# Kernel tuning notes

Hardware: AMD Instinct MI355X
Metric: run time of the kernel (lower is better)

## Reference

```python
import jax, jax.numpy as jnp
import numpy as np

EMBED_DIM = 768
NUM_HEADS = 12
HEAD_DIM = EMBED_DIM // NUM_HEADS
KERNEL = 7


def _neighbor_index(size, kernel):
    # NATTEN border-clamped neighborhood: window start = clip(i - k//2, 0, size-k)
    start = np.clip(np.arange(size) - kernel // 2, 0, size - kernel)
    return jnp.asarray(start[:, None] + np.arange(kernel)[None, :])  # [size, kernel]


def setup_inputs() -> dict:
    key = jax.random.key(0)
    k1, k2, k3, k4, k5 = jax.random.split(key, 5)
    B, H, W, C = 8, 64, 64, EMBED_DIM
    x = jax.random.normal(k1, (B, H, W, C), dtype=jnp.float32)
    # torch.nn.Linear layout: weight [out, in]
    w_qkv = jax.random.normal(k2, (3 * C, C), dtype=jnp.float32) * (C ** -0.5)
    b_qkv = jax.random.normal(k3, (3 * C,), dtype=jnp.float32) * 0.02
    w_proj = jax.random.normal(k4, (C, C), dtype=jnp.float32) * (C ** -0.5)
    b_proj = jax.random.normal(k5, (C,), dtype=jnp.float32) * 0.02
    return {"x": x, "w_qkv": w_qkv, "b_qkv": b_qkv, "w_proj": w_proj, "b_proj": b_proj}


def reference(x, w_qkv, b_qkv, w_proj, b_proj):
    B, H, W, C = x.shape
    scale = HEAD_DIM ** -0.5
    qkv = (x @ w_qkv.T + b_qkv).reshape(B, H, W, 3, NUM_HEADS, HEAD_DIM)
    q = qkv[..., 0, :, :] * scale          # [B,H,W,nh,hd]
    k = qkv[..., 1, :, :]
    v = qkv[..., 2, :, :]

    idx_i = _neighbor_index(H, KERNEL)      # [H,K]
    idx_j = _neighbor_index(W, KERNEL)      # [W,K]

    # Logits over the K*K local neighborhood, one shifted gather per offset
    # (avoids materializing [B,H,W,K2,nh,hd]).
    logits = []
    for ki in range(KERNEL):
        k_row = jnp.take(k, idx_i[:, ki], axis=1)          # [B,H,W,nh,hd]
        for kj in range(KERNEL):
            k_nb = jnp.take(k_row, idx_j[:, kj], axis=2)   # [B,H,W,nh,hd]
            logits.append(jnp.einsum('bhwnd,bhwnd->bhwn', q, k_nb))
    logits = jnp.stack(logits, axis=-1)                     # [B,H,W,nh,K2]
    attn = jax.nn.softmax(logits, axis=-1)

    out = jnp.zeros((B, H, W, NUM_HEADS, HEAD_DIM), dtype=x.dtype)
    off = 0
    for ki in range(KERNEL):
        v_row = jnp.take(v, idx_i[:, ki], axis=1)
        for kj in range(KERNEL):
            v_nb = jnp.take(v_row, idx_j[:, kj], axis=2)
            out = out + attn[..., off][..., None] * v_nb
            off += 1

    out = out.reshape(B, H, W, C)
    return out @ w_proj.T + b_proj
```

## Files before the change

### kernel.cpp

```cpp
#include <hip/hip_runtime.h>
#include <cstddef>

#define EMBED   768
#define NHEADS  12
#define HDIM    64
#define KSZ     7
#define IMG_H   64
#define IMG_W   64
#define BATCH   8
#define NTOK    (BATCH*IMG_H*IMG_W)
#define QKV_N   (3*EMBED)

typedef __attribute__((ext_vector_type(8))) short  bf16x8;
typedef __attribute__((ext_vector_type(4))) float  f32x4;
typedef __attribute__((ext_vector_type(8))) unsigned short u16x8;
typedef __attribute__((ext_vector_type(4))) unsigned short u16x4;

__device__ __forceinline__ unsigned short f2bf(float f) {
    unsigned int u = __float_as_uint(f);
    u += 0x7FFFu + ((u >> 16) & 1u);
    return (unsigned short)(u >> 16);
}

__device__ __forceinline__ void gload_lds16(const void* g, void* l) {
    __builtin_amdgcn_global_load_lds(
        (const __attribute__((address_space(1))) unsigned int*)g,
        (__attribute__((address_space(3))) unsigned int*)l, 16, 0, 0);
}

__global__ __launch_bounds__(256)
void cvt_bf16_kernel(const float* __restrict__ in, unsigned short* __restrict__ out, int n4)
{
    int i = blockIdx.x * 256 + threadIdx.x;
    if (i < n4) {
        float4 f = *(const float4*)(in + (size_t)i * 4);
        u16x4 o;
        o[0] = f2bf(f.x); o[1] = f2bf(f.y); o[2] = f2bf(f.z); o[3] = f2bf(f.w);
        *(u16x4*)(out + (size_t)i * 4) = o;
    }
}

template<int BF16OUT>
__global__ __launch_bounds__(512)
void gemm256(const unsigned short* __restrict__ A, const unsigned short* __restrict__ W,
             const float* __restrict__ bias, void* __restrict__ outp,
             int M, int N, int K, int scaleN, float scale)
{
    __shared__ unsigned short lds[65536];
    const int t_ = threadIdx.x;
    const int l = t_ & 63, w = t_ >> 6;
    const int wm = w >> 2, wn = w & 3;

    const int nby = N >> 8;
    const int xcd = blockIdx.x & 7;
    const int loc = blockIdx.x >> 3;
    const int bmg = loc / nby;
    int bnq = loc - bmg * nby;
    if (bmg & 1) bnq = nby - 1 - bnq;
    const int bm = (xcd * (((M >> 8) >> 3)) + bmg) << 8;
    const int bn = bnq << 8;

    const int kperm8 = ((l & 3) ^ ((l >> 3) & 3)) * 8;
    const unsigned short* gA = A + (size_t)(bm + 2 * w * 16 + (l >> 2)) * K + kperm8;
    const unsigned short* gB = W + (size_t)(bn + 2 * w * 16 + (l >> 2)) * K + kperm8;
    const size_t rstep = (size_t)16 * K;

    const int dA = w * 2048;
    const int foff = (l & 15) * 32 + (((l >> 4) ^ ((l >> 1) & 3)) * 8);
    const int aoff = wm * 8192;
    const int boff = 16384 + wn * 4096;

    f32x4 acc[8][4] = {};
    const int NT = K / 64;

#define BARRIER() asm volatile("s_barrier" ::: "memory")
#define WAITV4()  asm volatile("s_waitcnt vmcnt(4)" ::: "memory")
#define WAITV0()  asm volatile("s_waitcnt vmcnt(0)" ::: "memory")
#define STGA(c, k0, kk) do { \
        gload_lds16(gA + (size_t)(k0) + (kk) * 32,         lds + (c) + dA + (kk) * 512); \
        gload_lds16(gA + rstep + (size_t)(k0) + (kk) * 32, lds + (c) + dA + (2 + (kk)) * 512); } while (0)
#define STGB(c, k0, kk) do { \
        gload_lds16(gB + (size_t)(k0) + (kk) * 32,         lds + (c) + 16384 + dA + (kk) * 512); \
        gload_lds16(gB + rstep + (size_t)(k0) + (kk) * 32, lds + (c) + 16384 + dA + (2 + (kk)) * 512); } while (0)

    STGA(0, 0, 0); STGB(0, 0, 0); STGA(0, 0, 1); STGB(0, 0, 1);
    WAITV4();
    BARRIER();

    for (int t = 0; t < NT; ++t) {
        const int c  = (t & 1) << 15;
        const int cn = c ^ 32768;
        const int k1 = (t + 1) * 64;
        const bool pf = (t + 1) < NT;

        bf16x8 a[4], bq[4];

        #pragma unroll
        for (int m = 0; m < 4; ++m) a[m]  = *(const bf16x8*)(lds + c + aoff + (m * 2) * 512 + foff);
        #pragma unroll
        for (int n = 0; n < 4; ++n) bq[n] = *(const bf16x8*)(lds + c + boff + (n * 2) * 512 + foff);
        if (pf) STGA(cn, k1, 0);
        BARRIER();
        __builtin_amdgcn_s_setprio(1);
        #pragma unroll
        for (int m = 0; m < 4; ++m)
            #pragma unroll
            for (int n = 0; n < 4; ++n)
                acc[m][n] = __builtin_amdgcn_mfma_f32_16x16x32_bf16(a[m], bq[n], acc[m][n], 0, 0, 0);
        __builtin_amdgcn_s_setprio(0);

        #pragma unroll
        for (int m = 0; m < 4; ++m) a[m] = *(const bf16x8*)(lds + c + aoff + ((4 + m) * 2) * 512 + foff);
        if (pf) { STGB(cn, k1, 0); WAITV4(); } else { WAITV0(); }
        BARRIER();
        __builtin_amdgcn_s_setprio(1);
        #pragma unroll
        for (int m = 0; m < 4; ++m)
            #pragma unroll
            for (int n = 0; n < 4; ++n)
                acc[4 + m][n] = __builtin_amdgcn_mfma_f32_16x16x32_bf16(a[m], bq[n], acc[4 + m][n], 0, 0, 0);
        __builtin_amdgcn_s_setprio(0);

        #pragma unroll
        for (int m = 0; m < 4; ++m) a[m]  = *(const bf16x8*)(lds + c + aoff + (m * 2 + 1) * 512 + foff);
        #pragma unroll
        for (int n = 0; n < 4; ++n) bq[n] = *(const bf16x8*)(lds + c + boff + (n * 2 + 1) * 512 + foff);
        if (pf) STGA(cn, k1, 1);
        BARRIER();
        __builtin_amdgcn_s_setprio(1);
        #pragma unroll
        for (int m = 0; m < 4; ++m)
            #pragma unroll
            for (int n = 0; n < 4; ++n)
                acc[m][n] = __builtin_amdgcn_mfma_f32_16x16x32_bf16(a[m], bq[n], acc[m][n], 0, 0, 0);
        __builtin_amdgcn_s_setprio(0);

        #pragma unroll
        for (int m = 0; m < 4; ++m) a[m] = *(const bf16x8*)(lds + c + aoff + ((4 + m) * 2 + 1) * 512 + foff);
        if (pf) { STGB(cn, k1, 1); WAITV4(); }
        BARRIER();
        __builtin_amdgcn_s_setprio(1);
        #pragma unroll
        for (int m = 0; m < 4; ++m)
            #pragma unroll
            for (int n = 0; n < 4; ++n)
                acc[4 + m][n] = __builtin_amdgcn_mfma_f32_16x16x32_bf16(a[m], bq[n], acc[4 + m][n], 0, 0, 0);
        __builtin_amdgcn_s_setprio(0);
    }
#undef BARRIER
#undef WAITV4
#undef WAITV0
#undef STGA
#undef STGB

    const int cr = (l >> 4) * 4;
    const int cc = l & 15;
    #pragma unroll
    for (int m = 0; m < 8; ++m) {
        #pragma unroll
        for (int n = 0; n < 4; ++n) {
            const int col = bn + wn * 64 + n * 16 + cc;
            const float bv = bias[col];
            const bool sc = col < scaleN;
            #pragma unroll
            for (int r = 0; r < 4; ++r) {
                const int row = bm + wm * 128 + m * 16 + cr + r;
                float v = acc[m][n][r] + bv;
                if (sc) v *= scale;
                if (BF16OUT) ((unsigned short*)outp)[(size_t)row * N + col] = f2bf(v);
                else         ((float*)outp)[(size_t)row * N + col] = v;
            }
        }
    }
}

__global__ __launch_bounds__(256)
void natten_kernel(const unsigned short* __restrict__ qkv, unsigned short* __restrict__ attn_bf)
{
    __shared__ unsigned short smem[4 * 5888];
    const int t = threadIdx.x;
    const int w = t >> 6, l = t & 63;
    const int c15 = l & 15, g = l >> 4;
    const int blk = blockIdx.x;
    const int tg = blk & 15;
    const int h = (blk >> 4) % NHEADS;
    const int b = blk / (16 * NHEADS);
    const int ti = (tg >> 2) * 16, tj = (tg & 3) * 16;
    const int pi0 = ti + w * 4;
    const int ws = min(max(pi0 - 3, 0), IMG_H - 10);
    const int cs = min(max(tj - 3, 0), IMG_W - 22);
    const int pixbase = b * 4096;

    unsigned short* Kl = smem + w * 5888;
    unsigned short* Vt = Kl + 2304;

    const int pj = tj + c15;
    const int sj = min(max(pj - 3, 0), IMG_W - KSZ);
    const unsigned int cm = 0x7Fu << (sj - cs);
    unsigned int rm[4];
    #pragma unroll
    for (int qt = 0; qt < 4; ++qt) {
        int si = min(max(pi0 + qt - 3, 0), IMG_H - KSZ);
        rm[qt] = 0x7Fu << (si - ws);
    }

    bf16x8 qf[4][2];
    #pragma unroll
    for (int qt = 0; qt < 4; ++qt)
        #pragma unroll
        for (int dh = 0; dh < 2; ++dh)
            qf[qt][dh] = *(const bf16x8*)(qkv +
                (size_t)(pixbase + (pi0 + qt) * 64 + tj + c15) * QKV_N + h * HDIM + dh * 32 + g * 8);

    const int sr = l & 31;
    const int h5 = l >> 5;
    const int sig = ((sr & 12) << 1) | ((sr & 16) >> 2) | (sr & 3);

    u16x8 kst[4], vst[4];

    {
        int ur = sr / 22, uc = sr - ur * 22;
        int prow = min(ws + ur, IMG_H - 1);
        const u16x8* gk = (const u16x8*)(qkv +
            (size_t)(pixbase + prow * 64 + cs + uc) * QKV_N + EMBED + h * HDIM + h5 * 32);
        #pragma unroll
        for (int i = 0; i < 4; ++i) { kst[i] = gk[i]; vst[i] = gk[i + 96]; }
    }
    #pragma unroll
    for (int i = 0; i < 4; ++i) *(u16x8*)(Kl + sr * 72 + h5 * 32 + i * 8) = kst[i];
    #pragma unroll
    for (int i = 0; i < 4; ++i)
        #pragma unroll
        for (int e = 0; e < 8; ++e)
            Vt[(h5 * 32 + i * 8 + e) * 56 + sig] = vst[i][e];

    f32x4 oacc[4][4] = {};
    float spart[4] = {0.f, 0.f, 0.f, 0.f};

    #pragma unroll 1
    for (int C = 0; C < 7; ++C) {
        if (C < 6) {
            int kk = (C + 1) * 32 + sr;
            int ur = kk / 22, uc = kk - ur * 22;
            int prow = min(ws + ur, IMG_H - 1);
            const u16x8* gk = (const u16x8*)(qkv +
                (size_t)(pixbase + prow * 64 + cs + uc) * QKV_N + EMBED + h * HDIM + h5 * 32);
            #pragma unroll
            for (int i = 0; i < 4; ++i) { kst[i] = gk[i]; vst[i] = gk[i + 96]; }
        }

        bf16x8 ka[2][2], vb[4];
        #pragma unroll
        for (int kt = 0; kt < 2; ++kt)
            #pragma unroll
            for (int dh = 0; dh < 2; ++dh)
                ka[kt][dh] = *(const bf16x8*)(Kl + (kt * 16 + c15) * 72 + dh * 32 + g * 8);
        #pragma unroll
        for (int dt = 0; dt < 4; ++dt)
            vb[dt] = *(const bf16x8*)(Vt + (dt * 16 + c15) * 56 + g * 8);

        int kk0 = C * 32 + 4 * g;
        int a22 = kk0 / 22;
        int uc0 = kk0 - a22 * 22;
        int urx[2][4]; unsigned int cb[2][4];
        #pragma unroll
        for (int kt = 0; kt < 2; ++kt)
            #pragma unroll
            for (int r = 0; r < 4; ++r) {
                int x = uc0 + kt * 16 + r;
                int wrp = x >= 22;
                int uc = x - (wrp ? 22 : 0);
                urx[kt][r] = a22 + wrp;
                cb[kt][r] = (cm >> uc) & 1u;
            }

        #pragma unroll
        for (int qt = 0; qt < 4; ++qt) {
            f32x4 s0 = {}, s1 = {};
            s0 = __builtin_amdgcn_mfma_f32_16x16x32_bf16(ka[0][0], qf[qt][0], s0, 0, 0, 0);
            s0 = __builtin_amdgcn_mfma_f32_16x16x32_bf16(ka[0][1], qf[qt][1], s0, 0, 0, 0);
            s1 = __builtin_amdgcn_mfma_f32_16x16x32_bf16(ka[1][0], qf[qt][0], s1, 0, 0, 0);
            s1 = __builtin_amdgcn_mfma_f32_16x16x32_bf16(ka[1][1], qf[qt][1], s1, 0, 0, 0);
            float p[2][4];
            #pragma unroll
            for (int r = 0; r < 4; ++r) {
                float e0 = exp2f(s0[r]);
                float e1 = exp2f(s1[r]);
                p[0][r] = ((rm[qt] >> urx[0][r]) & cb[0][r]) ? e0 : 0.f;
                p[1][r] = ((rm[qt] >> urx[1][r]) & cb[1][r]) ? e1 : 0.f;
                spart[qt] += p[0][r] + p[1][r];
            }
            unsigned int pk[4];
            asm("v_cvt_pk_bf16_f32 %0, %1, %2" : "=v"(pk[0]) : "v"(p[0][0]), "v"(p[0][1]));
            asm("v_cvt_pk_bf16_f32 %0, %1, %2" : "=v"(pk[1]) : "v"(p[0][2]), "v"(p[0][3]));
            asm("v_cvt_pk_bf16_f32 %0, %1, %2" : "=v"(pk[2]) : "v"(p[1][0]), "v"(p[1][1]));
            asm("v_cvt_pk_bf16_f32 %0, %1, %2" : "=v"(pk[3]) : "v"(p[1][2]), "v"(p[1][3]));
            bf16x8 pa = *(bf16x8*)pk;
            #pragma unroll
            for (int dt = 0; dt < 4; ++dt)
                oacc[qt][dt] = __builtin_amdgcn_mfma_f32_16x16x32_bf16(pa, vb[dt], oacc[qt][dt], 0, 0, 0);
        }

        if (C < 6) {
            #pragma unroll
            for (int i = 0; i < 4; ++i) *(u16x8*)(Kl + sr * 72 + h5 * 32 + i * 8) = kst[i];
            #pragma unroll
            for (int i = 0; i < 4; ++i)
                #pragma unroll
                for (int e = 0; e < 8; ++e)
                    Vt[(h5 * 32 + i * 8 + e) * 56 + sig] = vst[i][e];
        }
    }

    #pragma unroll
    for (int qt = 0; qt < 4; ++qt) {
        float s = spart[qt];
        s += __shfl_xor(s, 16);
        s += __shfl_xor(s, 32);
        #pragma unroll
        for (int r = 0; r < 4; ++r) {
            float sb = __shfl(s, 4 * g + r);
            float inv = __builtin_amdgcn_rcpf(sb);
            size_t obase = (size_t)(pixbase + (pi0 + qt) * 64 + tj + 4 * g + r) * EMBED
                         + h * HDIM + c15;
            #pragma unroll
            for (int dt = 0; dt < 4; ++dt)
                attn_bf[obase + dt * 16] = f2bf(oacc[qt][dt][r] * inv);
        }
    }
}

extern "C" void kernel_launch(void* const* d_in, const int* in_sizes, int n_in,
                              void* d_out, int out_size, void* d_ws, size_t ws_size,
                              hipStream_t stream)
{
    const float* x      = (const float*)d_in[0];
    const float* w_qkv  = (const float*)d_in[1];
    const float* b_qkv  = (const float*)d_in[2];
    const float* w_proj = (const float*)d_in[3];
    const float* b_proj = (const float*)d_in[4];
    float* out = (float*)d_out;

    char* p = (char*)d_ws;
    unsigned short* qkv = (unsigned short*)p;     p += (size_t)NTOK * QKV_N * 2;
    unsigned short* xbf = (unsigned short*)p;
    unsigned short* attn_bf = xbf;                p += (size_t)NTOK * EMBED * 2;
    unsigned short* wq_bf = (unsigned short*)p;   p += (size_t)QKV_N * EMBED * 2;
    unsigned short* wp_bf = (unsigned short*)p;

    const float scale = 0.125f * 1.44269504088896f;

    {
        int n4 = NTOK * EMBED / 4;
        cvt_bf16_kernel<<<(n4 + 255) / 256, 256, 0, stream>>>(x, xbf, n4);
        n4 = QKV_N * EMBED / 4;
        cvt_bf16_kernel<<<(n4 + 255) / 256, 256, 0, stream>>>(w_qkv, wq_bf, n4);
        n4 = EMBED * EMBED / 4;
        cvt_bf16_kernel<<<(n4 + 255) / 256, 256, 0, stream>>>(w_proj, wp_bf, n4);
    }

    {
        gemm256<1><<<(NTOK / 256) * (QKV_N / 256), 512, 0, stream>>>(
            xbf, wq_bf, b_qkv, qkv, NTOK, QKV_N, EMBED, EMBED, scale);
    }

    natten_kernel<<<BATCH * NHEADS * 16, 256, 0, stream>>>(qkv, attn_bf);

    {
        gemm256<0><<<(NTOK / 256) * (EMBED / 256), 512, 0, stream>>>(
            attn_bf, wp_bf, b_proj, out, NTOK, EMBED, EMBED, 0, 1.0f);
    }
}
```

Before: 321.9 us.

## Stage GEMM epilogue through LDS for vectorized stores; merge bf16 conversion launches

The GEMM epilogue now writes bias-added results into a per-wave LDS scratch region and reads them back so each lane issues 16-byte row-contiguous global stores, replacing strided 2- or 4-byte scalar stores. The three fp32-to-bf16 conversion launches are merged into a single kernel that dispatches on the flat index. This is meant to improve write coalescing for the large QKV and output tensors and to cut launch overhead. The epilogue loop is not unrolled and reuses LDS without an explicit barrier after the main loop, which adds LDS traffic and a possible hazard with other waves' last tile reads.

```diff
diff --git a/kernel.cpp b/kernel.cpp
--- a/kernel.cpp
+++ b/kernel.cpp
@@ -29,15 +29,23 @@
 }
 
 __global__ __launch_bounds__(256)
-void cvt_bf16_kernel(const float* __restrict__ in, unsigned short* __restrict__ out, int n4)
+void cvt_all_kernel(const float* __restrict__ x, const float* __restrict__ wq,
+                    const float* __restrict__ wp, unsigned short* __restrict__ xbf,
+                    unsigned short* __restrict__ wqbf, unsigned short* __restrict__ wpbf)
 {
+    const int NX = NTOK * EMBED / 4;
+    const int NQ = QKV_N * EMBED / 4;
+    const int NP = EMBED * EMBED / 4;
     int i = blockIdx.x * 256 + threadIdx.x;
-    if (i < n4) {
-        float4 f = *(const float4*)(in + (size_t)i * 4);
-        u16x4 o;
-        o[0] = f2bf(f.x); o[1] = f2bf(f.y); o[2] = f2bf(f.z); o[3] = f2bf(f.w);
-        *(u16x4*)(out + (size_t)i * 4) = o;
-    }
+    const float* src; unsigned short* dst; int j;
+    if (i < NX)           { src = x;  dst = xbf;  j = i; }
+    else if (i < NX + NQ) { src = wq; dst = wqbf; j = i - NX; }
+    else if (i < NX + NQ + NP) { src = wp; dst = wpbf; j = i - NX - NQ; }
+    else return;
+    float4 f = *(const float4*)(src + (size_t)j * 4);
+    u16x4 o;
+    o[0] = f2bf(f.x); o[1] = f2bf(f.y); o[2] = f2bf(f.z); o[3] = f2bf(f.w);
+    *(u16x4*)(dst + (size_t)j * 4) = o;
 }
 
 template<int BF16OUT>
@@ -155,20 +163,48 @@
 
     const int cr = (l >> 4) * 4;
     const int cc = l & 15;
-    #pragma unroll
-    for (int m = 0; m < 8; ++m) {
-        #pragma unroll
-        for (int n = 0; n < 4; ++n) {
-            const int col = bn + wn * 64 + n * 16 + cc;
-            const float bv = bias[col];
-            const bool sc = col < scaleN;
-            #pragma unroll
-            for (int r = 0; r < 4; ++r) {
-                const int row = bm + wm * 128 + m * 16 + cr + r;
-                float v = acc[m][n][r] + bv;
-                if (sc) v *= scale;
-                if (BF16OUT) ((unsigned short*)outp)[(size_t)row * N + col] = f2bf(v);
-                else         ((float*)outp)[(size_t)row * N + col] = v;
+    const int colbase = bn + wn * 64;
+
+    if (BF16OUT) {
+        unsigned short* eb = lds + w * 2048;
+        unsigned short* out16 = (unsigned short*)outp;
+        #pragma unroll 1
+        for (int m = 0; m < 8; ++m) {
+            #pragma unroll
+            for (int n = 0; n < 4; ++n) {
+                const int col = colbase + n * 16 + cc;
+                const float bv = bias[col];
+                const bool sc = col < scaleN;
+                #pragma unroll
+                for (int r = 0; r < 4; ++r) {
+                    float v = acc[m][n][r] + bv;
+                    if (sc) v *= scale;
+                    eb[(cr + r) * 64 + n * 16 + cc] = f2bf(v);
+                }
+            }
+            const int rowg = bm + wm * 128 + m * 16;
+            u16x8 v0 = *(const u16x8*)(eb + l * 8);
+            u16x8 v1 = *(const u16x8*)(eb + 512 + l * 8);
+            *(u16x8*)(out16 + (size_t)(rowg + (l >> 3)) * N + colbase + (l & 7) * 8) = v0;
+            *(u16x8*)(out16 + (size_t)(rowg + 8 + (l >> 3)) * N + colbase + (l & 7) * 8) = v1;
+        }
+    } else {
+        float* ebf = (float*)(void*)lds + w * 1024;
+        float* outf = (float*)outp;
+        #pragma unroll 1
+        for (int m = 0; m < 8; ++m) {
+            #pragma unroll
+            for (int n = 0; n < 4; ++n) {
+                const float bv = bias[colbase + n * 16 + cc];
+                #pragma unroll
+                for (int r = 0; r < 4; ++r)
+                    ebf[(cr + r) * 64 + n * 16 + cc] = acc[m][n][r] + bv;
+            }
+            const int rowg = bm + wm * 128 + m * 16;
+            #pragma unroll
+            for (int s = 0; s < 4; ++s) {
+                f32x4 v = *(const f32x4*)(ebf + s * 256 + l * 4);
+                *(f32x4*)(outf + (size_t)(rowg + s * 4 + (l >> 4)) * N + colbase + (l & 15) * 4) = v;
             }
         }
     }
@@ -351,12 +387,9 @@
     const float scale = 0.125f * 1.44269504088896f;
 
     {
-        int n4 = NTOK * EMBED / 4;
-        cvt_bf16_kernel<<<(n4 + 255) / 256, 256, 0, stream>>>(x, xbf, n4);
-        n4 = QKV_N * EMBED / 4;
-        cvt_bf16_kernel<<<(n4 + 255) / 256, 256, 0, stream>>>(w_qkv, wq_bf, n4);
-        n4 = EMBED * EMBED / 4;
-        cvt_bf16_kernel<<<(n4 + 255) / 256, 256, 0, stream>>>(w_proj, wp_bf, n4);
+        const int ntot = (NTOK * EMBED + QKV_N * EMBED + EMBED * EMBED) / 4;
+        cvt_all_kernel<<<(ntot + 255) / 256, 256, 0, stream>>>(
+            x, w_qkv, w_proj, xbf, wq_bf, wp_bf);
     }
 
     {
```

Result: slower. 507.7 us (+57.7%).

## Use 4-stage K=32 LDS pipeline in GEMM and merge bf16 conversion launches

Applied to the files above, without the earlier changes.

The GEMM main loop moves from a double-buffered K=64 tile with split A/B staging to a four-buffer ring of K=32 tiles, prefetching three tiles ahead and issuing A and B loads together. Deeper prefetch is meant to hide more global-to-LDS latency, at the cost of more loop iterations and barriers per unit of work. The three fp32-to-bf16 conversion launches are also fused into a single kernel, which removes launch overhead.

```diff
diff --git a/kernel.cpp b/kernel.cpp
--- a/kernel.cpp
+++ b/kernel.cpp
@@ -29,15 +29,23 @@
 }
 
 __global__ __launch_bounds__(256)
-void cvt_bf16_kernel(const float* __restrict__ in, unsigned short* __restrict__ out, int n4)
+void cvt_all_kernel(const float* __restrict__ x, const float* __restrict__ wq,
+                    const float* __restrict__ wp, unsigned short* __restrict__ xbf,
+                    unsigned short* __restrict__ wqbf, unsigned short* __restrict__ wpbf)
 {
+    const int NX = NTOK * EMBED / 4;
+    const int NQ = QKV_N * EMBED / 4;
+    const int NP = EMBED * EMBED / 4;
     int i = blockIdx.x * 256 + threadIdx.x;
-    if (i < n4) {
-        float4 f = *(const float4*)(in + (size_t)i * 4);
-        u16x4 o;
-        o[0] = f2bf(f.x); o[1] = f2bf(f.y); o[2] = f2bf(f.z); o[3] = f2bf(f.w);
-        *(u16x4*)(out + (size_t)i * 4) = o;
-    }
+    const float* src; unsigned short* dst; int j;
+    if (i < NX)           { src = x;  dst = xbf;  j = i; }
+    else if (i < NX + NQ) { src = wq; dst = wqbf; j = i - NX; }
+    else if (i < NX + NQ + NP) { src = wp; dst = wpbf; j = i - NX - NQ; }
+    else return;
+    float4 f = *(const float4*)(src + (size_t)j * 4);
+    u16x4 o;
+    o[0] = f2bf(f.x); o[1] = f2bf(f.y); o[2] = f2bf(f.z); o[3] = f2bf(f.w);
+    *(u16x4*)(dst + (size_t)j * 4) = o;
 }
 
 template<int BF16OUT>
@@ -61,45 +69,40 @@
     const int bn = bnq << 8;
 
     const int kperm8 = ((l & 3) ^ ((l >> 3) & 3)) * 8;
-    const unsigned short* gA = A + (size_t)(bm + 2 * w * 16 + (l >> 2)) * K + kperm8;
-    const unsigned short* gB = W + (size_t)(bn + 2 * w * 16 + (l >> 2)) * K + kperm8;
-    const size_t rstep = (size_t)16 * K;
-
-    const int dA = w * 2048;
+    const unsigned short* gA = A + (size_t)(bm + w * 16 + (l >> 2)) * K + kperm8;
+    const unsigned short* gB = W + (size_t)(bn + w * 16 + (l >> 2)) * K + kperm8;
+    const size_t rstep = (size_t)128 * K;
+
     const int foff = (l & 15) * 32 + (((l >> 4) ^ ((l >> 1) & 3)) * 8);
-    const int aoff = wm * 8192;
-    const int boff = 16384 + wn * 4096;
+    const int aoff = wm * 8 * 512;
+    const int boff = 8192 + wn * 4 * 512;
 
     f32x4 acc[8][4] = {};
-    const int NT = K / 64;
+    const int NT = K / 32;
 
 #define BARRIER() asm volatile("s_barrier" ::: "memory")
+#define WAITV8()  asm volatile("s_waitcnt vmcnt(8)" ::: "memory")
 #define WAITV4()  asm volatile("s_waitcnt vmcnt(4)" ::: "memory")
 #define WAITV0()  asm volatile("s_waitcnt vmcnt(0)" ::: "memory")
-#define STGA(c, k0, kk) do { \
-        gload_lds16(gA + (size_t)(k0) + (kk) * 32,         lds + (c) + dA + (kk) * 512); \
-        gload_lds16(gA + rstep + (size_t)(k0) + (kk) * 32, lds + (c) + dA + (2 + (kk)) * 512); } while (0)
-#define STGB(c, k0, kk) do { \
-        gload_lds16(gB + (size_t)(k0) + (kk) * 32,         lds + (c) + 16384 + dA + (kk) * 512); \
-        gload_lds16(gB + rstep + (size_t)(k0) + (kk) * 32, lds + (c) + 16384 + dA + (2 + (kk)) * 512); } while (0)
-
-    STGA(0, 0, 0); STGB(0, 0, 0); STGA(0, 0, 1); STGB(0, 0, 1);
-    WAITV4();
+#define STG(tt) do { \
+        const int cc_ = ((tt) & 3) * 16384; const size_t ko_ = (size_t)(tt) * 32; \
+        gload_lds16(gA + ko_,         lds + cc_ + w * 512); \
+        gload_lds16(gA + rstep + ko_, lds + cc_ + (w + 8) * 512); \
+        gload_lds16(gB + ko_,         lds + cc_ + 8192 + w * 512); \
+        gload_lds16(gB + rstep + ko_, lds + cc_ + 8192 + (w + 8) * 512); } while (0)
+
+    STG(0); STG(1); STG(2);
+    WAITV8();
     BARRIER();
 
     for (int t = 0; t < NT; ++t) {
-        const int c  = (t & 1) << 15;
-        const int cn = c ^ 32768;
-        const int k1 = (t + 1) * 64;
-        const bool pf = (t + 1) < NT;
-
+        const int c = (t & 3) * 16384;
         bf16x8 a[4], bq[4];
 
         #pragma unroll
-        for (int m = 0; m < 4; ++m) a[m]  = *(const bf16x8*)(lds + c + aoff + (m * 2) * 512 + foff);
-        #pragma unroll
-        for (int n = 0; n < 4; ++n) bq[n] = *(const bf16x8*)(lds + c + boff + (n * 2) * 512 + foff);
-        if (pf) STGA(cn, k1, 0);
+        for (int m = 0; m < 4; ++m) a[m]  = *(const bf16x8*)(lds + c + aoff + m * 512 + foff);
+        #pragma unroll
+        for (int n = 0; n < 4; ++n) bq[n] = *(const bf16x8*)(lds + c + boff + n * 512 + foff);
         BARRIER();
         __builtin_amdgcn_s_setprio(1);
         #pragma unroll
@@ -110,8 +113,10 @@
         __builtin_amdgcn_s_setprio(0);
 
         #pragma unroll
-        for (int m = 0; m < 4; ++m) a[m] = *(const bf16x8*)(lds + c + aoff + ((4 + m) * 2) * 512 + foff);
-        if (pf) { STGB(cn, k1, 0); WAITV4(); } else { WAITV0(); }
+        for (int m = 0; m < 4; ++m) a[m] = *(const bf16x8*)(lds + c + aoff + (4 + m) * 512 + foff);
+        if (t + 3 < NT)      { STG(t + 3); WAITV8(); }
+        else if (t == NT - 3)  WAITV4();
+        else if (t == NT - 2)  WAITV0();
         BARRIER();
         __builtin_amdgcn_s_setprio(1);
         #pragma unroll
@@ -120,38 +125,12 @@
             for (int n = 0; n < 4; ++n)
                 acc[4 + m][n] = __builtin_amdgcn_mfma_f32_16x16x32_bf16(a[m], bq[n], acc[4 + m][n], 0, 0, 0);
         __builtin_amdgcn_s_setprio(0);
-
-        #pragma unroll
-        for (int m = 0; m < 4; ++m) a[m]  = *(const bf16x8*)(lds + c + aoff + (m * 2 + 1) * 512 + foff);
-        #pragma unroll
-        for (int n = 0; n < 4; ++n) bq[n] = *(const bf16x8*)(lds + c + boff + (n * 2 + 1) * 512 + foff);
-        if (pf) STGA(cn, k1, 1);
-        BARRIER();
-        __builtin_amdgcn_s_setprio(1);
-        #pragma unroll
-        for (int m = 0; m < 4; ++m)
-            #pragma unroll
-            for (int n = 0; n < 4; ++n)
-                acc[m][n] = __builtin_amdgcn_mfma_f32_16x16x32_bf16(a[m], bq[n], acc[m][n], 0, 0, 0);
-        __builtin_amdgcn_s_setprio(0);
-
-        #pragma unroll
-        for (int m = 0; m < 4; ++m) a[m] = *(const bf16x8*)(lds + c + aoff + ((4 + m) * 2 + 1) * 512 + foff);
-        if (pf) { STGB(cn, k1, 1); WAITV4(); }
-        BARRIER();
-        __builtin_amdgcn_s_setprio(1);
-        #pragma unroll
-        for (int m = 0; m < 4; ++m)
-            #pragma unroll
-            for (int n = 0; n < 4; ++n)
-                acc[4 + m][n] = __builtin_amdgcn_mfma_f32_16x16x32_bf16(a[m], bq[n], acc[4 + m][n], 0, 0, 0);
-        __builtin_amdgcn_s_setprio(0);
     }
 #undef BARRIER
+#undef WAITV8
 #undef WAITV4
 #undef WAITV0
-#undef STGA
-#undef STGB
+#undef STG
 
     const int cr = (l >> 4) * 4;
     const int cc = l & 15;
@@ -351,12 +330,9 @@
     const float scale = 0.125f * 1.44269504088896f;
 
     {
-        int n4 = NTOK * EMBED / 4;
-        cvt_bf16_kernel<<<(n4 + 255) / 256, 256, 0, stream>>>(x, xbf, n4);
-        n4 = QKV_N * EMBED / 4;
-        cvt_bf16_kernel<<<(n4 + 255) / 256, 256, 0, stream>>>(w_qkv, wq_bf, n4);
-        n4 = EMBED * EMBED / 4;
-        cvt_bf16_kernel<<<(n4 + 255) / 256, 256, 0, stream>>>(w_proj, wp_bf, n4);
+        const int ntot = (NTOK * EMBED + QKV_N * EMBED + EMBED * EMBED) / 4;
+        cvt_all_kernel<<<(ntot + 255) / 256, 256, 0, stream>>>(
+            x, w_qkv, w_proj, xbf, wq_bf, wp_bf);
     }
 
     {
```

New measurement: 315.3 us (median of 2 runs). 2.1% less time.
